# Kernel tuning notes

Measured on AMD Instinct MI355X. Metric: run time of the kernel, lower is better.

The kernel has to match this reference:

```python
import jax, jax.numpy as jnp
import numpy as np

NEG_SLOPE = 0.2  # PyG GATConv default
LN_EPS = 1e-5

B, N, DIN, H, DH, DOUT = 256, 256, 128, 4, 32, 1


def setup_inputs() -> dict:
    key = jax.random.key(0)
    ks = jax.random.split(key, 12)
    s = lambda *shape: 0.1
    return {
        "x": jax.random.normal(ks[0], (B, N, DIN), jnp.float32),
        "adj": jnp.ones((B, N, N), jnp.float32),  # unused (graph is fully connected)
        # GATConv 1: dim_in -> H heads x DH
        "W1": jax.random.normal(ks[1], (DIN, H * DH), jnp.float32) * 0.05,
        "b1": jnp.zeros((H * DH,), jnp.float32),
        "att_src1": jax.random.normal(ks[2], (H, DH), jnp.float32) * 0.1,
        "att_dst1": jax.random.normal(ks[3], (H, DH), jnp.float32) * 0.1,
        # LayerNorm over hidden dim H*DH
        "gamma": jnp.ones((H * DH,), jnp.float32),
        "beta": jnp.zeros((H * DH,), jnp.float32),
        # GATConv 2: H*DH -> 1 head x DOUT, concat=False
        "W2": jax.random.normal(ks[4], (H * DH, DOUT), jnp.float32) * 0.05,
        "b2": jnp.zeros((DOUT,), jnp.float32),
        "att_src2": jax.random.normal(ks[5], (1, DOUT), jnp.float32) * 0.1,
        "att_dst2": jax.random.normal(ks[6], (1, DOUT), jnp.float32) * 0.1,
    }


def _gat_layer(x, W, b, att_src, att_dst):
    """Dense GATConv on a fully-connected graph.
    x: [B, N, Fin] -> out: [B, N, H, D], attn: [B, H, N, N].
    Node i aggregates over all j: e_ij = leaky_relu(a_dst.h_i + a_src.h_j).
    """
    Hh, D = att_src.shape
    h = (x @ W).reshape(x.shape[0], x.shape[1], Hh, D)          # [B,N,H,D]
    a_src = jnp.einsum("bnhd,hd->bnh", h, att_src)              # neighbor term
    a_dst = jnp.einsum("bnhd,hd->bnh", h, att_dst)              # central term
    e = a_dst.transpose(0, 2, 1)[:, :, :, None] + a_src.transpose(0, 2, 1)[:, :, None, :]  # [B,H,N,N]
    e = jax.nn.leaky_relu(e, NEG_SLOPE)
    attn = jax.nn.softmax(e, axis=-1)                           # softmax over neighbors j
    out = jnp.einsum("bhij,bjhd->bihd", attn, h)                # [B,N,H,D]
    return out, attn, b


def reference(x, adj, W1, b1, att_src1, att_dst1, gamma, beta, W2, b2, att_src2, att_dst2):
    del adj  # module ignores adj; graph is fully connected
    # layer 1: concat heads
    h1, _, _ = _gat_layer(x, W1, b1, att_src1, att_dst1)
    h1 = h1.reshape(B, N, H * DH) + b1                          # [B,N,H*DH]
    # LayerNorm over hidden dim
    mu = jnp.mean(h1, axis=-1, keepdims=True)
    var = jnp.mean(jnp.square(h1 - mu), axis=-1, keepdims=True)
    h1 = (h1 - mu) * jax.lax.rsqrt(var + LN_EPS) * gamma + beta
    # layer 2: single head, concat=False (mean over 1 head == identity)
    h2, attn2, _ = _gat_layer(h1, W2, b2, att_src2, att_dst2)
    h2 = h2.reshape(B, N, DOUT) + b2
    out = jax.nn.elu(h2)                                        # [B,N,DOUT]
    return out
```

## Files before the change

### kernel.cpp

```cpp
#include <hip/hip_runtime.h>
#include <hip/hip_bf16.h>
#include <math.h>

#define BB 256
#define NN 256
#define DIN 128
#define NH 4
#define DH 32
#define HID 128
#define NEG 0.2f
#define LN_EPS 1e-5f
#define L2E 1.44269504f

typedef __attribute__((ext_vector_type(8))) short short8;
typedef __attribute__((ext_vector_type(4))) float float4v;
typedef __attribute__((ext_vector_type(2))) unsigned int uint2v;
typedef __attribute__((ext_vector_type(4))) unsigned int uint4v;

__device__ __forceinline__ short f2bs(float f) {
    return (short)((__float_as_uint(f) + 0x8000u) >> 16);
}
__device__ __forceinline__ unsigned int pack2(float a, float b) {
    return __builtin_amdgcn_perm(__float_as_uint(b) + 0x8000u,
                                 __float_as_uint(a) + 0x8000u, 0x07060302u);
}

#define MFMA16(a, b, c) __builtin_amdgcn_mfma_f32_16x16x32_bf16(a, b, c, 0, 0, 0)

__global__ __launch_bounds__(1024, 4) void k_mega(
    const float* __restrict__ x, const float* __restrict__ W1,
    const float* __restrict__ as1, const float* __restrict__ ad1,
    const float* __restrict__ b1, const float* __restrict__ gamma,
    const float* __restrict__ beta, const float* __restrict__ W2,
    const float* __restrict__ bias2, const float* __restrict__ att_src2,
    const float* __restrict__ att_dst2, float* __restrict__ out)
{
    const int b = blockIdx.x, t = threadIdx.x;
    const int w = t >> 6, lane = t & 63;
    const int l16 = lane & 15, q = lane >> 4;

    __shared__ short uA[34816];
    __shared__ short W1Ts[128 * 136];
    __shared__ short awT[16 * 136];
    __shared__ float Bs[NH][NN], Bsp[NH][NN];
    __shared__ float ssraw[NH][NN], ddlog[NH][NN];
    __shared__ float b1s[HID], gws[HID], bws[HID];
    __shared__ float part[NH][NN * 3];
    __shared__ float Ssc[2];
    __shared__ float h2v[NN], Ej[NN], Epj[NN];

    const float* xb = x + (size_t)b * NN * DIN;
#pragma unroll
    for (int it = 0; it < 8; ++it) {
        const int idx = t + it * 1024;
        const int row = idx >> 5, c4 = idx & 31;
        const float4v v = ((const float4v*)xb)[idx];
        uint2v p;
        p[0] = pack2(v[0], v[1]);
        p[1] = pack2(v[2], v[3]);
        *(uint2v*)&uA[row * 136 + c4 * 4] = p;
    }
    {
        const int n = t & 127, kc = t >> 7, k0 = kc * 16;
        float v[16];
#pragma unroll
        for (int e = 0; e < 16; ++e) v[e] = W1[(k0 + e) * HID + n];
        uint4v pa, pb;
#pragma unroll
        for (int e = 0; e < 4; ++e) {
            pa[e] = pack2(v[2 * e], v[2 * e + 1]);
            pb[e] = pack2(v[8 + 2 * e], v[9 + 2 * e]);
        }
        *(uint4v*)&W1Ts[n * 136 + k0] = pa;
        *(uint4v*)&W1Ts[n * 136 + k0 + 8] = pb;
    }
    {
        const int rr = t >> 7, k = t & 127;
        const int hh = rr & 3;
        const float* att = ((rr & 4) ? ad1 : as1) + hh * 32;
        const float* wrow = W1 + k * HID + hh * 32;
        float acc = 0.f;
#pragma unroll
        for (int e = 0; e < 8; ++e) {
            const float4v wv = *(const float4v*)(wrow + e * 4);
            const float4v av = *(const float4v*)(att + e * 4);
            acc += wv[0] * av[0] + wv[1] * av[1] + wv[2] * av[2] + wv[3] * av[3];
        }
        awT[rr * 136 + k] = f2bs(acc * L2E);
    }
    if (t < HID) {
        b1s[t] = b1[t];
        const float w2v = W2[t];
        gws[t] = gamma[t] * w2v;
        bws[t] = beta[t] * w2v;
    }
    __syncthreads();

    const int dtile = w & 7, jhalf = w >> 3;
    const bool isaug = (w == 0) || (w == 15);
    float4v acc1[8], accA[8];
#pragma unroll
    for (int i = 0; i < 8; ++i) {
        acc1[i] = (float4v){0.f, 0.f, 0.f, 0.f};
        accA[i] = (float4v){0.f, 0.f, 0.f, 0.f};
    }
    const short* arow = &W1Ts[(dtile * 16 + l16) * 136];
    const short* arow2 = &awT[l16 * 136];
#pragma unroll
    for (int ks = 0; ks < 4; ++ks) {
        const short8 afr = *(const short8*)&arow[ks * 32 + q * 8];
        short8 afr2;
        if (isaug) afr2 = *(const short8*)&arow2[ks * 32 + q * 8];
#pragma unroll
        for (int nt = 0; nt < 8; ++nt) {
            const short8 bfr = *(const short8*)&uA[((jhalf * 8 + nt) * 16 + l16) * 136 + ks * 32 + q * 8];
            acc1[nt] = MFMA16(afr, bfr, acc1[nt]);
            if (isaug) accA[nt] = MFMA16(afr2, bfr, accA[nt]);
        }
    }
    if (isaug && q < 2) {
        float (*dstA)[NN] = (q == 0) ? ssraw : ddlog;
#pragma unroll
        for (int nt = 0; nt < 8; ++nt)
#pragma unroll
            for (int r = 0; r < 4; ++r)
                dstA[r][jhalf * 128 + nt * 16 + l16] = accA[nt][r];
    }
    __syncthreads();
#pragma unroll
    for (int nt = 0; nt < 8; ++nt)
#pragma unroll
        for (int r = 0; r < 4; ++r)
            uA[(dtile * 16 + q * 4 + r) * 264 + (jhalf * 8 + nt) * 16 + l16] = f2bs(acc1[nt][r]);
    {
        const int hs = t >> 8, js = t & 255;
        const float vs = ssraw[hs][js];
        Bs[hs][js] = exp2f(vs);
        Bsp[hs][js] = exp2f(NEG * vs);
    }
    __syncthreads();

    {
        if (w < 2) {
            const float* src = (w == 0) ? gws : bws;
            float v = src[lane] + src[lane + 64];
#pragma unroll
            for (int m = 1; m < 64; m <<= 1) v += __shfl_xor(v, m, 64);
            if (lane == 0) Ssc[w] = v;
        }
        const int hh = w >> 2, qtr = w & 3;
        float Au[4], Apu[4];
#pragma unroll
        for (int u = 0; u < 4; ++u) {
            const float dv = ddlog[hh][qtr * 64 + u * 16 + l16];
            Au[u] = exp2f(dv);
            Apu[u] = exp2f(NEG * dv);
        }
        float4v acc2[4][2], accL[4];
#pragma unroll
        for (int u = 0; u < 4; ++u) {
            acc2[u][0] = (float4v){0.f, 0.f, 0.f, 0.f};
            acc2[u][1] = (float4v){0.f, 0.f, 0.f, 0.f};
            accL[u]    = (float4v){0.f, 0.f, 0.f, 0.f};
        }
        short8 ones;
#pragma unroll
        for (int e = 0; e < 8; ++e) ones[e] = (short)0x3F80;

        const short* hTh = &uA[(hh * 32) * 264];
#pragma unroll 2
        for (int ks = 0; ks < 8; ++ks) {
            const short8 a0 = *(const short8*)&hTh[l16 * 264 + ks * 32 + q * 8];
            const short8 a1 = *(const short8*)&hTh[(16 + l16) * 264 + ks * 32 + q * 8];
            const float4v bs0 = *(const float4v*)&Bs[hh][ks * 32 + q * 8];
            const float4v bs1 = *(const float4v*)&Bs[hh][ks * 32 + q * 8 + 4];
            const float4v bp0 = *(const float4v*)&Bsp[hh][ks * 32 + q * 8];
            const float4v bp1 = *(const float4v*)&Bsp[hh][ks * 32 + q * 8 + 4];
            const float bsj[8] = {bs0[0], bs0[1], bs0[2], bs0[3], bs1[0], bs1[1], bs1[2], bs1[3]};
            const float bpj[8] = {bp0[0], bp0[1], bp0[2], bp0[3], bp1[0], bp1[1], bp1[2], bp1[3]};
#pragma unroll
            for (int u = 0; u < 4; ++u) {
                union { short8 s8; unsigned int u32[4]; } bfr;
#pragma unroll
                for (int p = 0; p < 4; ++p) {
                    const float w0 = fmaxf(Au[u] * bsj[2 * p],     Apu[u] * bpj[2 * p]);
                    const float w1 = fmaxf(Au[u] * bsj[2 * p + 1], Apu[u] * bpj[2 * p + 1]);
                    bfr.u32[p] = pack2(w0, w1);
                }
                acc2[u][0] = MFMA16(a0, bfr.s8, acc2[u][0]);
                acc2[u][1] = MFMA16(a1, bfr.s8, acc2[u][1]);
                accL[u]    = MFMA16(ones, bfr.s8, accL[u]);
            }
        }
        float b1r[8], gwr[8];
#pragma unroll
        for (int mt = 0; mt < 2; ++mt)
#pragma unroll
            for (int r = 0; r < 4; ++r) {
                const int d = hh * 32 + mt * 16 + q * 4 + r;
                b1r[mt * 4 + r] = b1s[d];
                gwr[mt * 4 + r] = gws[d];
            }
#pragma unroll
        for (int u = 0; u < 4; ++u) {
            const float inv = 1.f / accL[u][0];
            float s = 0.f, sq = 0.f, t3 = 0.f;
#pragma unroll
            for (int mt = 0; mt < 2; ++mt)
#pragma unroll
                for (int r = 0; r < 4; ++r) {
                    const float v = fmaf(acc2[u][mt][r], inv, b1r[mt * 4 + r]);
                    s += v;
                    sq = fmaf(v, v, sq);
                    t3 = fmaf(v, gwr[mt * 4 + r], t3);
                }
            s  += __shfl_xor(s, 16, 64);  s  += __shfl_xor(s, 32, 64);
            sq += __shfl_xor(sq, 16, 64); sq += __shfl_xor(sq, 32, 64);
            t3 += __shfl_xor(t3, 16, 64); t3 += __shfl_xor(t3, 32, 64);
            if (q == 0) {
                float* pp = &part[hh][(qtr * 64 + u * 16 + l16) * 3];
                pp[0] = s; pp[1] = sq; pp[2] = t3;
            }
        }
    }
    __syncthreads();

    if (t < NN) {
        float s = 0.f, sq = 0.f, t3 = 0.f;
#pragma unroll
        for (int hh2 = 0; hh2 < 4; ++hh2) {
            const float* pp = &part[hh2][t * 3];
            s += pp[0]; sq += pp[1]; t3 += pp[2];
        }
        const float mu = s * (1.f / HID);
        const float var = sq * (1.f / HID) - mu * mu;
        const float rs = rsqrtf(var + LN_EPS);
        const float h2 = rs * (t3 - mu * Ssc[0]) + Ssc[1];
        h2v[t] = h2;
        const float e = h2 * att_src2[0];
        Ej[t]  = __expf(e);
        Epj[t] = __expf(NEG * e);
    }
    __syncthreads();

    {
        const int i3 = t & 255, hf = t >> 8;
        const float ed = h2v[i3] * att_dst2[0];
        const float Di = __expf(ed), Dip = __expf(NEG * ed);
        float l2 = 0.f, num = 0.f;
#pragma unroll 4
        for (int jz = 0; jz < 64; ++jz) {
            const int j = hf * 64 + jz;
            const float wgt = fmaxf(Di * Ej[j], Dip * Epj[j]);
            l2 += wgt;
            num = fmaf(wgt, h2v[j], num);
        }
        float* pw = &part[0][0];
        const int pb = (hf * 256 + i3) * 2;
        pw[pb] = l2; pw[pb + 1] = num;
        __syncthreads();
        if (hf == 0) {
#pragma unroll
            for (int k = 1; k < 4; ++k) {
                const int pk = (k * 256 + i3) * 2;
                l2 += pw[pk]; num += pw[pk + 1];
            }
            float o = num / l2 + bias2[0];
            o = (o > 0.f) ? o : (__expf(o) - 1.f);
            out[b * NN + i3] = o;
        }
    }
}

extern "C" void kernel_launch(void* const* d_in, const int* in_sizes, int n_in,
                              void* d_out, int out_size, void* d_ws, size_t ws_size,
                              hipStream_t stream) {
    const float* x   = (const float*)d_in[0];
    const float* W1  = (const float*)d_in[2];
    const float* b1  = (const float*)d_in[3];
    const float* as1 = (const float*)d_in[4];
    const float* ad1 = (const float*)d_in[5];
    const float* gam = (const float*)d_in[6];
    const float* bet = (const float*)d_in[7];
    const float* W2  = (const float*)d_in[8];
    const float* bi2 = (const float*)d_in[9];
    const float* as2 = (const float*)d_in[10];
    const float* ad2 = (const float*)d_in[11];
    float* out = (float*)d_out;

    k_mega<<<BB, 1024, 0, stream>>>(x, W1, as1, ad1, b1, gam, bet, W2,
                                    bi2, as2, ad2, out);
}
```

Before: 146.4 us.

## Precompute W1 bf16 transpose in prep kernel and refactor leaky-relu softmax weights

```diff
diff --git a/kernel.cpp b/kernel.cpp
--- a/kernel.cpp
+++ b/kernel.cpp
@@ -27,9 +27,36 @@
 
 #define MFMA16(a, b, c) __builtin_amdgcn_mfma_f32_16x16x32_bf16(a, b, c, 0, 0, 0)
 
+__global__ __launch_bounds__(256) void k_prep(
+    const float* __restrict__ W1, const float* __restrict__ as1,
+    const float* __restrict__ ad1, short* __restrict__ W1Tg,
+    short* __restrict__ awTg)
+{
+    const int blk = blockIdx.x;
+    if (blk < 64) {
+        const int idx = blk * 256 + threadIdx.x;
+        const int n = idx >> 7, k = idx & 127;
+        W1Tg[idx] = f2bs(W1[k * HID + n]);
+    } else {
+        const int id = (blk - 64) * 256 + threadIdx.x;
+        const int rr = id >> 7, k = id & 127;
+        const int hh = rr & 3;
+        const float* att = ((rr & 4) ? ad1 : as1) + hh * 32;
+        const float* wrow = W1 + k * HID + hh * 32;
+        float acc = 0.f;
+#pragma unroll
+        for (int e = 0; e < 8; ++e) {
+            const float4v wv = *(const float4v*)(wrow + e * 4);
+            const float4v av = *(const float4v*)(att + e * 4);
+            acc += wv[0] * av[0] + wv[1] * av[1] + wv[2] * av[2] + wv[3] * av[3];
+        }
+        awTg[rr * DIN + k] = f2bs(acc * L2E);
+    }
+}
+
 __global__ __launch_bounds__(1024, 4) void k_mega(
-    const float* __restrict__ x, const float* __restrict__ W1,
-    const float* __restrict__ as1, const float* __restrict__ ad1,
+    const float* __restrict__ x, const short* __restrict__ W1Tg,
+    const short* __restrict__ awTg,
     const float* __restrict__ b1, const float* __restrict__ gamma,
     const float* __restrict__ beta, const float* __restrict__ W2,
     const float* __restrict__ bias2, const float* __restrict__ att_src2,
@@ -42,12 +69,15 @@
     __shared__ short uA[34816];
     __shared__ short W1Ts[128 * 136];
     __shared__ short awT[16 * 136];
-    __shared__ float Bs[NH][NN], Bsp[NH][NN];
+    __shared__ float Sj[NH][NN] __attribute__((aligned(16)));
+    __shared__ float Bpj[NH][NN] __attribute__((aligned(16)));
     __shared__ float ssraw[NH][NN], ddlog[NH][NN];
     __shared__ float b1s[HID], gws[HID], bws[HID];
     __shared__ float part[NH][NN * 3];
     __shared__ float Ssc[2];
-    __shared__ float h2v[NN], Ej[NN], Epj[NN];
+    __shared__ float h2v[NN] __attribute__((aligned(16)));
+    __shared__ float Tjt[NN] __attribute__((aligned(16)));
+    __shared__ float Ept[NN] __attribute__((aligned(16)));
 
     const float* xb = x + (size_t)b * NN * DIN;
 #pragma unroll
@@ -61,32 +91,15 @@
         *(uint2v*)&uA[row * 136 + c4 * 4] = p;
     }
     {
-        const int n = t & 127, kc = t >> 7, k0 = kc * 16;
-        float v[16];
-#pragma unroll
-        for (int e = 0; e < 16; ++e) v[e] = W1[(k0 + e) * HID + n];
-        uint4v pa, pb;
-#pragma unroll
-        for (int e = 0; e < 4; ++e) {
-            pa[e] = pack2(v[2 * e], v[2 * e + 1]);
-            pb[e] = pack2(v[8 + 2 * e], v[9 + 2 * e]);
-        }
-        *(uint4v*)&W1Ts[n * 136 + k0] = pa;
-        *(uint4v*)&W1Ts[n * 136 + k0 + 8] = pb;
+        const int n = t >> 3, k0 = (t & 7) * 16;
+        const uint4v a = *(const uint4v*)&W1Tg[n * DIN + k0];
+        const uint4v c = *(const uint4v*)&W1Tg[n * DIN + k0 + 8];
+        *(uint4v*)&W1Ts[n * 136 + k0] = a;
+        *(uint4v*)&W1Ts[n * 136 + k0 + 8] = c;
     }
     {
         const int rr = t >> 7, k = t & 127;
-        const int hh = rr & 3;
-        const float* att = ((rr & 4) ? ad1 : as1) + hh * 32;
-        const float* wrow = W1 + k * HID + hh * 32;
-        float acc = 0.f;
-#pragma unroll
-        for (int e = 0; e < 8; ++e) {
-            const float4v wv = *(const float4v*)(wrow + e * 4);
-            const float4v av = *(const float4v*)(att + e * 4);
-            acc += wv[0] * av[0] + wv[1] * av[1] + wv[2] * av[2] + wv[3] * av[3];
-        }
-        awT[rr * 136 + k] = f2bs(acc * L2E);
+        awT[rr * 136 + k] = awTg[rr * DIN + k];
     }
     if (t < HID) {
         b1s[t] = b1[t];
@@ -135,8 +148,8 @@
     {
         const int hs = t >> 8, js = t & 255;
         const float vs = ssraw[hs][js];
-        Bs[hs][js] = exp2f(vs);
-        Bsp[hs][js] = exp2f(NEG * vs);
+        Sj[hs][js]  = exp2f(0.8f * vs);
+        Bpj[hs][js] = exp2f(0.2f * vs);
     }
     __syncthreads();
 
@@ -149,13 +162,10 @@
             if (lane == 0) Ssc[w] = v;
         }
         const int hh = w >> 2, qtr = w & 3;
-        float Au[4], Apu[4];
-#pragma unroll
-        for (int u = 0; u < 4; ++u) {
-            const float dv = ddlog[hh][qtr * 64 + u * 16 + l16];
-            Au[u] = exp2f(dv);
-            Apu[u] = exp2f(NEG * dv);
-        }
+        float R[4];
+#pragma unroll
+        for (int u = 0; u < 4; ++u)
+            R[u] = exp2f(0.8f * ddlog[hh][qtr * 64 + u * 16 + l16]);
         float4v acc2[4][2], accL[4];
 #pragma unroll
         for (int u = 0; u < 4; ++u) {
@@ -166,27 +176,26 @@
         short8 ones;
 #pragma unroll
         for (int e = 0; e < 8; ++e) ones[e] = (short)0x3F80;
+        const float4v one4 = {1.f, 1.f, 1.f, 1.f};
 
         const short* hTh = &uA[(hh * 32) * 264];
 #pragma unroll 2
         for (int ks = 0; ks < 8; ++ks) {
             const short8 a0 = *(const short8*)&hTh[l16 * 264 + ks * 32 + q * 8];
             const short8 a1 = *(const short8*)&hTh[(16 + l16) * 264 + ks * 32 + q * 8];
-            const float4v bs0 = *(const float4v*)&Bs[hh][ks * 32 + q * 8];
-            const float4v bs1 = *(const float4v*)&Bs[hh][ks * 32 + q * 8 + 4];
-            const float4v bp0 = *(const float4v*)&Bsp[hh][ks * 32 + q * 8];
-            const float4v bp1 = *(const float4v*)&Bsp[hh][ks * 32 + q * 8 + 4];
-            const float bsj[8] = {bs0[0], bs0[1], bs0[2], bs0[3], bs1[0], bs1[1], bs1[2], bs1[3]};
-            const float bpj[8] = {bp0[0], bp0[1], bp0[2], bp0[3], bp1[0], bp1[1], bp1[2], bp1[3]};
+            const float4v s0 = *(const float4v*)&Sj[hh][ks * 32 + q * 8];
+            const float4v s1 = *(const float4v*)&Sj[hh][ks * 32 + q * 8 + 4];
+            const float4v p0 = *(const float4v*)&Bpj[hh][ks * 32 + q * 8];
+            const float4v p1 = *(const float4v*)&Bpj[hh][ks * 32 + q * 8 + 4];
 #pragma unroll
             for (int u = 0; u < 4; ++u) {
+                const float4v m0 = __builtin_elementwise_max(R[u] * s0, one4) * p0;
+                const float4v m1 = __builtin_elementwise_max(R[u] * s1, one4) * p1;
                 union { short8 s8; unsigned int u32[4]; } bfr;
-#pragma unroll
-                for (int p = 0; p < 4; ++p) {
-                    const float w0 = fmaxf(Au[u] * bsj[2 * p],     Apu[u] * bpj[2 * p]);
-                    const float w1 = fmaxf(Au[u] * bsj[2 * p + 1], Apu[u] * bpj[2 * p + 1]);
-                    bfr.u32[p] = pack2(w0, w1);
-                }
+                bfr.u32[0] = pack2(m0.x, m0.y);
+                bfr.u32[1] = pack2(m0.z, m0.w);
+                bfr.u32[2] = pack2(m1.x, m1.y);
+                bfr.u32[3] = pack2(m1.z, m1.w);
                 acc2[u][0] = MFMA16(a0, bfr.s8, acc2[u][0]);
                 acc2[u][1] = MFMA16(a1, bfr.s8, acc2[u][1]);
                 accL[u]    = MFMA16(ones, bfr.s8, accL[u]);
@@ -238,23 +247,29 @@
         const float h2 = rs * (t3 - mu * Ssc[0]) + Ssc[1];
         h2v[t] = h2;
         const float e = h2 * att_src2[0];
-        Ej[t]  = __expf(e);
-        Epj[t] = __expf(NEG * e);
+        Tjt[t] = __expf(0.8f * e);
+        Ept[t] = __expf(0.2f * e);
     }
     __syncthreads();
 
     {
         const int i3 = t & 255, hf = t >> 8;
         const float ed = h2v[i3] * att_dst2[0];
-        const float Di = __expf(ed), Dip = __expf(NEG * ed);
-        float l2 = 0.f, num = 0.f;
+        const float Q = __expf(0.8f * ed);
+        const float4v one4 = {1.f, 1.f, 1.f, 1.f};
+        float4v l4 = {0.f, 0.f, 0.f, 0.f}, n4 = {0.f, 0.f, 0.f, 0.f};
 #pragma unroll 4
-        for (int jz = 0; jz < 64; ++jz) {
-            const int j = hf * 64 + jz;
-            const float wgt = fmaxf(Di * Ej[j], Dip * Epj[j]);
-            l2 += wgt;
-            num = fmaf(wgt, h2v[j], num);
-        }
+        for (int jz = 0; jz < 16; ++jz) {
+            const int j4 = (hf * 16 + jz) * 4;
+            const float4v tv = *(const float4v*)&Tjt[j4];
+            const float4v ev = *(const float4v*)&Ept[j4];
+            const float4v hv = *(const float4v*)&h2v[j4];
+            const float4v w4 = __builtin_elementwise_max(Q * tv, one4) * ev;
+            l4 += w4;
+            n4 += w4 * hv;
+        }
+        float l2  = (l4.x + l4.y) + (l4.z + l4.w);
+        float num = (n4.x + n4.y) + (n4.z + n4.w);
         float* pw = &part[0][0];
         const int pb = (hf * 256 + i3) * 2;
         pw[pb] = l2; pw[pb + 1] = num;
@@ -288,6 +303,10 @@
     const float* ad2 = (const float*)d_in[11];
     float* out = (float*)d_out;
 
-    k_mega<<<BB, 1024, 0, stream>>>(x, W1, as1, ad1, b1, gam, bet, W2,
+    short* W1Tg = (short*)d_ws;
+    short* awTg = (short*)d_ws + DIN * HID;
+
+    k_prep<<<68, 256, 0, stream>>>(W1, as1, ad1, W1Tg, awTg);
+    k_mega<<<BB, 1024, 0, stream>>>(x, W1Tg, awTg, b1, gam, bet, W2,
                                     bi2, as2, ad2, out);
 }
```

Result: no change. 147.3 us (+0.6%).
